# Optimization experiments

Hardware: AMD Instinct MI355X
Metric: run time of the kernel (lower is better)

Reference implementation:

```python
import jax, jax.numpy as jnp
import numpy as np

B, C, H = 16, 256, 32          # batch, in_channels(=out_channels), image_size
HEADS, HS = 8, 32              # heads = out_channels // head_size
D = HEADS * HS                 # head_dim = 256
N = H * H                      # tokens = 1024
EPS = 1e-5


def _rel_indices(h, w):
    # Faithful port of RelativeAttention2d.get_indices
    y = np.arange(h)
    x = np.arange(w)
    y1, x1, y2, x2 = np.meshgrid(y, x, y, x, indexing='ij')
    idx = (y1 - y2 + h - 1) * (2 * w - 1) + (x1 - x2 + w - 1)
    return jnp.asarray(idx.reshape(-1), dtype=jnp.int32)  # [N*N]


def setup_inputs() -> dict:
    key = jax.random.key(0)
    ks = jax.random.split(key, 10)
    s = 0.02
    return {
        'x': jax.random.normal(ks[0], (B, C, H, H), jnp.float32),
        'ln_g': jnp.ones((C,), jnp.float32),
        'ln_b': jnp.zeros((C,), jnp.float32),
        'wq': jax.random.normal(ks[1], (D, C), jnp.float32) * s,
        'bq': jnp.zeros((D,), jnp.float32),
        'wk': jax.random.normal(ks[2], (D, C), jnp.float32) * s,
        'bk': jnp.zeros((D,), jnp.float32),
        'wv': jax.random.normal(ks[3], (D, C), jnp.float32) * s,
        'bv': jnp.zeros((D,), jnp.float32),
        'wo': jax.random.normal(ks[4], (C, D), jnp.float32) * s,
        'bo': jnp.zeros((C,), jnp.float32),
        'rel_bias': jax.random.normal(ks[5], (HEADS, (2 * H - 1) * (2 * H - 1)), jnp.float32),
        'rel_idx': _rel_indices(H, H),
    }


def reference(x, ln_g, ln_b, wq, bq, wk, bk, wv, bv, wo, bo, rel_bias, rel_idx):
    b = x.shape[0]
    # norm(): LayerNorm over channel axis (dim 1 after the double transpose)
    mu = jnp.mean(x, axis=1, keepdims=True)
    var = jnp.mean((x - mu) ** 2, axis=1, keepdims=True)
    xn = (x - mu) / jnp.sqrt(var + EPS)
    xn = xn * ln_g[None, :, None, None] + ln_b[None, :, None, None]
    # reshape_for_linear: raw reshape [b, C, H, W] -> [b, N, C] (as in torch)
    xr = xn.reshape(b, N, C)
    # projections, then raw view(b, heads, head_size, -1) as in torch
    q = (xr @ wq.T + bq).reshape(b, HEADS, HS, N)
    k = (xr @ wk.T + bk).reshape(b, HEADS, HS, N)
    v = (xr @ wv.T + bv).reshape(b, HEADS, HS, N)
    # dots = k^T q / sqrt(head_dim)   [b, heads, N, N]
    dots = jnp.einsum('bhdn,bhdm->bhnm', k, q) / np.float32(np.sqrt(D))
    # gathered relative position bias  [heads, N, N]
    bias = rel_bias[:, rel_idx].reshape(HEADS, N, N)
    attn = jax.nn.softmax(dots + bias[None], axis=-2)  # non-standard softmax dim
    # out = v @ attn  [b, heads, head_size, N]
    out = jnp.einsum('bhdn,bhnm->bhdm', v, attn)
    out = out.reshape(b, H, H, D)  # raw view as in torch
    out = out @ wo.T + bo          # to_output linear (dropout is identity in eval)
    out = out.reshape(b, C, H, H)  # raw view back to [b, out_channels, H, W]
    return x + out
```

## Files before the change

### kernel.cpp

```cpp
#include <hip/hip_runtime.h>
#include <cstdint>

#define PERB 262144

typedef __attribute__((ext_vector_type(8))) short bf16x8;
typedef __attribute__((ext_vector_type(4))) float f32x4;
typedef unsigned short ushort_t;

__device__ __forceinline__ uint16_t f2bf(float f) {
    uint32_t u = __float_as_uint(f);
    u += 0x7fff + ((u >> 16) & 1);
    return (uint16_t)(u >> 16);
}

__global__ __launch_bounds__(256) void wcvt_kernel(
    const float* __restrict__ wq, const float* __restrict__ wk,
    const float* __restrict__ wv, const float* __restrict__ wo,
    ushort_t* __restrict__ oq, ushort_t* __restrict__ ok,
    ushort_t* __restrict__ ov, ushort_t* __restrict__ oo)
{
    const int which = blockIdx.x >> 6;
    const int idx = ((blockIdx.x & 63) * 256 + threadIdx.x) * 4;
    const float* src = which == 0 ? wq : which == 1 ? wk : which == 2 ? wv : wo;
    ushort_t* dst    = which == 0 ? oq : which == 1 ? ok : which == 2 ? ov : oo;
    const float4 v = *(const float4*)&src[idx];
    uint2 p;
    p.x = (uint32_t)f2bf(v.x) | ((uint32_t)f2bf(v.y) << 16);
    p.y = (uint32_t)f2bf(v.z) | ((uint32_t)f2bf(v.w) << 16);
    *(uint2*)&dst[idx] = p;
}

__global__ __launch_bounds__(256) void ln_kernel(
    const float* __restrict__ x, const float* __restrict__ gam,
    const float* __restrict__ bet, ushort_t* __restrict__ X)
{
    const int blk = blockIdx.x;
    const int b   = blk >> 4;
    const int sp0 = (blk & 15) << 6;
    const int tid = threadIdx.x;
    const int spl = tid & 63;
    const int cg  = tid >> 6;
    const int c0  = cg << 6;
    const int sp  = sp0 + spl;
    const float* xb = x + (size_t)b * PERB + sp;

    float vals[64];
    float s = 0.f, sq = 0.f;
#pragma unroll
    for (int i = 0; i < 64; ++i) {
        float v = xb[(size_t)(c0 + i) * 1024];
        vals[i] = v; s += v; sq += v * v;
    }
    __shared__ float rs[4][64];
    __shared__ float rq[4][64];
    rs[cg][spl] = s; rq[cg][spl] = sq;
    __syncthreads();
    const float ts = rs[0][spl] + rs[1][spl] + rs[2][spl] + rs[3][spl];
    const float tq = rq[0][spl] + rq[1][spl] + rq[2][spl] + rq[3][spl];
    const float mean = ts * (1.f / 256.f);
    const float var  = tq * (1.f / 256.f) - mean * mean;
    const float rstd = rsqrtf(var + 1e-5f);

    ushort_t* Xb = X + (size_t)b * PERB + sp;
#pragma unroll
    for (int i = 0; i < 64; ++i) {
        const int c = c0 + i;
        Xb[(size_t)c * 1024] = f2bf((vals[i] - mean) * rstd * gam[c] + bet[c]);
    }
}

__global__ __launch_bounds__(256, 3) void qkv_kernel(
    const ushort_t* __restrict__ X,
    const ushort_t* __restrict__ wq, const float* __restrict__ bq,
    const ushort_t* __restrict__ wk, const float* __restrict__ bk,
    const ushort_t* __restrict__ wv, const float* __restrict__ bv,
    ushort_t* __restrict__ Q, ushort_t* __restrict__ K, ushort_t* __restrict__ V)
{
    __shared__ __align__(16) ushort_t Xl[512 * 8];
    __shared__ __align__(16) ushort_t Wl[3][512 * 8];

    const int blk = blockIdx.x;
    const int m0  = (blk >> 2) << 6;
    const int n0  = (blk & 3) << 6;
    const int tid = threadIdx.x;
    const int w    = tid >> 6;
    const int lane = tid & 63;
    const int quad = lane >> 4;
    const int c    = lane & 15;

    f32x4 acc[3][4];
#pragma unroll
    for (int o3 = 0; o3 < 3; ++o3)
#pragma unroll
        for (int i = 0; i < 4; ++i) acc[o3][i] = (f32x4){0.f, 0.f, 0.f, 0.f};

    for (int kc = 0; kc < 4; ++kc) {
        const int k0 = kc << 6;
        __syncthreads();
#pragma unroll
        for (int i = 0; i < 2; ++i) {
            const int id = tid + i * 256;
            const int kq = id >> 6, m = id & 63;
            *(bf16x8*)&Xl[id * 8] = *(const bf16x8*)&X[(size_t)(m0 + m) * 256 + k0 + kq * 8];
        }
#pragma unroll
        for (int i = 0; i < 2; ++i) {
            const int id = tid + i * 256;
            const int kq = id >> 6, n = id & 63;
            const size_t g = (size_t)(n0 + n) * 256 + k0 + kq * 8;
            *(bf16x8*)&Wl[0][id * 8] = *(const bf16x8*)&wq[g];
            *(bf16x8*)&Wl[1][id * 8] = *(const bf16x8*)&wk[g];
            *(bf16x8*)&Wl[2][id * 8] = *(const bf16x8*)&wv[g];
        }
        __syncthreads();
#pragma unroll
        for (int ks = 0; ks < 2; ++ks) {
            const int kq = ks * 4 + quad;
            bf16x8 af[4];
#pragma unroll
            for (int msub = 0; msub < 4; ++msub)
                af[msub] = *(const bf16x8*)&Xl[(kq * 64 + msub * 16 + c) * 8];
            bf16x8 bw[3];
#pragma unroll
            for (int o3 = 0; o3 < 3; ++o3)
                bw[o3] = *(const bf16x8*)&Wl[o3][(kq * 64 + w * 16 + c) * 8];
#pragma unroll
            for (int o3 = 0; o3 < 3; ++o3)
#pragma unroll
                for (int msub = 0; msub < 4; ++msub)
                    acc[o3][msub] = __builtin_amdgcn_mfma_f32_16x16x32_bf16(
                        bw[o3], af[msub], acc[o3][msub], 0, 0, 0);
        }
    }

    const int n = n0 + w * 16 + quad * 4;
    const float4 bq4 = *(const float4*)&bq[n];
    const float4 bk4 = *(const float4*)&bk[n];
    const float4 bv4 = *(const float4*)&bv[n];
    ushort_t* outs[3] = {Q, K, V};
    const float4 bias[3] = {bq4, bk4, bv4};
#pragma unroll
    for (int msub = 0; msub < 4; ++msub) {
        const size_t m = (size_t)(m0 + msub * 16 + c);
#pragma unroll
        for (int o3 = 0; o3 < 3; ++o3) {
            const f32x4 a = acc[o3][msub];
            uint2 p;
            p.x = (uint32_t)f2bf(a[0] + bias[o3].x) | ((uint32_t)f2bf(a[1] + bias[o3].y) << 16);
            p.y = (uint32_t)f2bf(a[2] + bias[o3].z) | ((uint32_t)f2bf(a[3] + bias[o3].w) << 16);
            *(uint2*)&outs[o3][m * 256 + n] = p;
        }
    }
}

#define C1F 0.09016844005556022f
#define LOG2EF 1.4426950408889634f

__global__ __launch_bounds__(256, 4) void attn_kernel(
    const ushort_t* __restrict__ Q, const ushort_t* __restrict__ K,
    const ushort_t* __restrict__ V, const float* __restrict__ relb,
    ushort_t* __restrict__ O)
{
    __shared__ __align__(16) unsigned char smem[28672];
    char* Pb = (char*)smem;
    char* Kl = (char*)(smem + 16384);
    char* Vl = (char*)(smem + 20480);

    const int blk = blockIdx.x;
    const int bh  = blk & 127;
    const int mt  = blk >> 7;
    const int b   = bh >> 3;
    const int h   = bh & 7;
    const int m0  = mt << 7;
    const int tid = threadIdx.x;
    const int w    = tid >> 6;
    const int lane = tid & 63;
    const int quad = lane >> 4;
    const int c    = lane & 15;

    const size_t base = (size_t)b * PERB + (size_t)h * 32768;
    const ushort_t* Qg = Q + base;
    const ushort_t* Kg = K + base;
    const ushort_t* Vg = V + base;
    const float* rbh = relb + h * 3969;

    {
        const int mm = tid & 127;
        const int sg = tid >> 7;
        union { bf16x8 v; uint16_t u[8]; } g0, g1;
#pragma unroll
        for (int j = 0; j < 8; ++j)
            g0.u[j] = Qg[(size_t)(sg * 16 + j) * 1024 + m0 + mm];
#pragma unroll
        for (int j = 0; j < 8; ++j)
            g1.u[j] = Qg[(size_t)(sg * 16 + 8 + j) * 1024 + m0 + mm];
        *(bf16x8*)(Pb + (sg * 2 + 0) * 2048 + mm * 16) = g0.v;
        *(bf16x8*)(Pb + (sg * 2 + 1) * 2048 + mm * 16) = g1.v;
    }
    __syncthreads();
    bf16x8 qfrag[8];
#pragma unroll
    for (int msub = 0; msub < 8; ++msub)
        qfrag[msub] = *(const bf16x8*)(Pb + quad * 2048 + (msub * 16 + c) * 16);

    int moff[8];
#pragma unroll
    for (int msub = 0; msub < 8; ++msub) {
        const int m = m0 + msub * 16 + c;
        moff[msub] = 1984 - (m >> 5) * 63 - (m & 31);
    }

    f32x4 oacc[2][2], dacc[2];
#pragma unroll
    for (int i = 0; i < 2; ++i) {
        dacc[i] = (f32x4){0.f, 0.f, 0.f, 0.f};
#pragma unroll
        for (int j = 0; j < 2; ++j) oacc[i][j] = (f32x4){0.f, 0.f, 0.f, 0.f};
    }
    bf16x8 onesf;
#pragma unroll
    for (int j = 0; j < 8; ++j) onesf[j] = (short)0x3F80;

    const int knn = tid & 63, ksg = tid >> 6;
    const int vs  = tid >> 3, vng = tid & 7;
    const int kWr = ksg * 1024 + knn * 16;
    const int vWr = vs * 128 + ((vng ^ (vs & 7)) << 4);
    const int kRd = quad * 1024 + (w * 16 + c) * 16;
    const int pWr = c * 128 + (((2 * w + (quad >> 1)) ^ (c & 7)) << 4) + ((quad & 1) << 3);
    const int c7  = c & 7;

    uint32_t kpre[8]; bf16x8 vpre;
#pragma unroll
    for (int j = 0; j < 8; ++j) kpre[j] = Kg[(size_t)(ksg * 8 + j) * 1024 + knn];
    vpre = *(const bf16x8*)&Vg[(size_t)vs * 1024 + vng * 8];

    for (int ch = 0; ch < 16; ++ch) {
        const int n0c = ch << 6;
        const int cb  = ch & 1;

        {
            uint4 kp;
            kp.x = kpre[0] | (kpre[1] << 16);
            kp.y = kpre[2] | (kpre[3] << 16);
            kp.z = kpre[4] | (kpre[5] << 16);
            kp.w = kpre[6] | (kpre[7] << 16);
            *(uint4*)(Kl + kWr) = kp;
            *(bf16x8*)(Vl + cb * 4096 + vWr) = vpre;
        }
        __syncthreads();

        {
            const int n0n = ((ch + 1) & 15) << 6;
#pragma unroll
            for (int j = 0; j < 8; ++j)
                kpre[j] = Kg[(size_t)(ksg * 8 + j) * 1024 + n0n + knn];
            vpre = *(const bf16x8*)&Vg[(size_t)vs * 1024 + n0n + vng * 8];
        }

        const bf16x8 kf = *(const bf16x8*)(Kl + kRd);
        f32x4 sacc[8];
#pragma unroll
        for (int msub = 0; msub < 8; ++msub) {
            const f32x4 z = {0.f, 0.f, 0.f, 0.f};
            sacc[msub] = __builtin_amdgcn_mfma_f32_16x16x32_bf16(kf, qfrag[msub], z, 0, 0, 0);
        }

        const int nbase = n0c + w * 16 + quad * 4;
        const int nidx0 = (nbase >> 5) * 63 + (nbase & 31);
#pragma unroll
        for (int msub = 0; msub < 8; ++msub) {
            const float* bp = rbh + nidx0 + moff[msub];
            float p[4];
#pragma unroll
            for (int r = 0; r < 4; ++r)
                p[r] = __builtin_amdgcn_exp2f(fmaf(bp[r], LOG2EF, sacc[msub][r] * C1F));
            uint2 pk;
            pk.x = __builtin_amdgcn_perm(__float_as_uint(p[1]), __float_as_uint(p[0]), 0x07060302u);
            pk.y = __builtin_amdgcn_perm(__float_as_uint(p[3]), __float_as_uint(p[2]), 0x07060302u);
            *(uint2*)(Pb + msub * 2048 + pWr) = pk;
        }
        __syncthreads();

#pragma unroll
        for (int kstep = 0; kstep < 2; ++kstep) {
            const int u = ((kstep * 4 + quad) ^ c7) << 4;
            const bf16x8 vf0 = *(const bf16x8*)(Vl + cb * 4096 + c * 128 + u);
            const bf16x8 vf1 = *(const bf16x8*)(Vl + cb * 4096 + (16 + c) * 128 + u);
#pragma unroll
            for (int mi = 0; mi < 2; ++mi) {
                const bf16x8 pf = *(const bf16x8*)(Pb + ((w * 2 + mi) * 16 + c) * 128 + u);
                oacc[0][mi] = __builtin_amdgcn_mfma_f32_16x16x32_bf16(vf0, pf, oacc[0][mi], 0, 0, 0);
                oacc[1][mi] = __builtin_amdgcn_mfma_f32_16x16x32_bf16(vf1, pf, oacc[1][mi], 0, 0, 0);
                dacc[mi]    = __builtin_amdgcn_mfma_f32_16x16x32_bf16(onesf, pf, dacc[mi], 0, 0, 0);
            }
        }
    }

    ushort_t* Ob = O + base;
#pragma unroll
    for (int mi = 0; mi < 2; ++mi) {
        const float inv = 1.0f / dacc[mi][0];
        const int m = m0 + (w * 2 + mi) * 16 + c;
#pragma unroll
        for (int ssub = 0; ssub < 2; ++ssub)
#pragma unroll
            for (int r = 0; r < 4; ++r)
                Ob[(size_t)(ssub * 16 + quad * 4 + r) * 1024 + m] = f2bf(oacc[ssub][mi][r] * inv);
    }
}

__global__ __launch_bounds__(256, 4) void oproj_kernel(
    const ushort_t* __restrict__ A, const ushort_t* __restrict__ wo,
    const float* __restrict__ bo, const float* __restrict__ x,
    float* __restrict__ out)
{
    __shared__ __align__(16) ushort_t Al[512 * 8];
    __shared__ __align__(16) ushort_t Wl[512 * 8];

    const int blk = blockIdx.x;
    const int m0  = (blk >> 2) << 6;
    const int n0  = (blk & 3) << 6;
    const int tid = threadIdx.x;
    const int w    = tid >> 6;
    const int lane = tid & 63;
    const int quad = lane >> 4;
    const int c    = lane & 15;

    f32x4 acc[4];
#pragma unroll
    for (int i = 0; i < 4; ++i) acc[i] = (f32x4){0.f, 0.f, 0.f, 0.f};

    for (int kc = 0; kc < 4; ++kc) {
        const int k0 = kc << 6;
        __syncthreads();
#pragma unroll
        for (int i = 0; i < 2; ++i) {
            const int id = tid + i * 256;
            const int kq = id >> 6, mn = id & 63;
            *(bf16x8*)&Al[id * 8] = *(const bf16x8*)&A [(size_t)(m0 + mn) * 256 + k0 + kq * 8];
            *(bf16x8*)&Wl[id * 8] = *(const bf16x8*)&wo[(size_t)(n0 + mn) * 256 + k0 + kq * 8];
        }
        __syncthreads();
#pragma unroll
        for (int ks = 0; ks < 2; ++ks) {
            const int kq = ks * 4 + quad;
            const bf16x8 bw = *(const bf16x8*)&Wl[(kq * 64 + w * 16 + c) * 8];
#pragma unroll
            for (int msub = 0; msub < 4; ++msub) {
                const bf16x8 af = *(const bf16x8*)&Al[(kq * 64 + msub * 16 + c) * 8];
                acc[msub] = __builtin_amdgcn_mfma_f32_16x16x32_bf16(bw, af, acc[msub], 0, 0, 0);
            }
        }
    }

    const int n = n0 + w * 16 + quad * 4;
    const float4 bo4 = *(const float4*)&bo[n];
#pragma unroll
    for (int msub = 0; msub < 4; ++msub) {
        const size_t g = (size_t)(m0 + msub * 16 + c) * 256 + n;
        const float4 r = *(const float4*)&x[g];
        float4 t;
        t.x = acc[msub][0] + bo4.x + r.x;
        t.y = acc[msub][1] + bo4.y + r.y;
        t.z = acc[msub][2] + bo4.z + r.z;
        t.w = acc[msub][3] + bo4.w + r.w;
        *(float4*)&out[g] = t;
    }
}

extern "C" void kernel_launch(void* const* d_in, const int* in_sizes, int n_in,
                              void* d_out, int out_size, void* d_ws, size_t ws_size,
                              hipStream_t stream)
{
    (void)in_sizes; (void)n_in; (void)out_size; (void)ws_size;
    const float* x   = (const float*)d_in[0];
    const float* lng = (const float*)d_in[1];
    const float* lnb = (const float*)d_in[2];
    const float* wq  = (const float*)d_in[3];
    const float* bq  = (const float*)d_in[4];
    const float* wk  = (const float*)d_in[5];
    const float* bk  = (const float*)d_in[6];
    const float* wv  = (const float*)d_in[7];
    const float* bv  = (const float*)d_in[8];
    const float* wo  = (const float*)d_in[9];
    const float* bo  = (const float*)d_in[10];
    const float* rb  = (const float*)d_in[11];

    ushort_t* ws = (ushort_t*)d_ws;
    ushort_t* Xbf = ws;
    ushort_t* Qbf = ws + 1 * 4194304;
    ushort_t* Kbf = ws + 2 * 4194304;
    ushort_t* Vbf = ws + 3 * 4194304;
    ushort_t* Obf = ws + 4 * 4194304;
    ushort_t* Wqb = ws + 5 * 4194304;
    ushort_t* Wkb = Wqb + 65536;
    ushort_t* Wvb = Wkb + 65536;
    ushort_t* Wob = Wvb + 65536;
    float* out = (float*)d_out;

    hipLaunchKernelGGL(wcvt_kernel,  dim3(256),  dim3(256), 0, stream,
                       wq, wk, wv, wo, Wqb, Wkb, Wvb, Wob);
    hipLaunchKernelGGL(ln_kernel,    dim3(256),  dim3(256), 0, stream, x, lng, lnb, Xbf);
    hipLaunchKernelGGL(qkv_kernel,   dim3(1024), dim3(256), 0, stream,
                       Xbf, Wqb, bq, Wkb, bk, Wvb, bv, Qbf, Kbf, Vbf);
    hipLaunchKernelGGL(attn_kernel,  dim3(1024), dim3(256), 0, stream, Qbf, Kbf, Vbf, rb, Obf);
    hipLaunchKernelGGL(oproj_kernel, dim3(1024), dim3(256), 0, stream, Obf, Wob, bo, x, out);
}
```

Measured before the change: 175.7 us.

## Vectorize LayerNorm and drop LDS staging in QKV and output projection GEMMs

LayerNorm now uses 512 blocks. Each thread loads float4 spans of four spatial positions over eight channels, reduces across 32 channel groups in shared memory, and writes ushort4. This targets more memory-level parallelism and wider accesses. The QKV and output projection GEMMs no longer stage tiles through LDS with barriers. Each wave loads its MFMA operands straight from global memory (relying on cache reuse), which removes the syncs and LDS traffic but adds redundant global loads. The QKV kernel's occupancy hint rises from 3 to 4.

```diff
diff --git a/kernel.cpp b/kernel.cpp
--- a/kernel.cpp
+++ b/kernel.cpp
@@ -30,55 +30,72 @@
     *(uint2*)&dst[idx] = p;
 }
 
-__global__ __launch_bounds__(256) void ln_kernel(
+__global__ __launch_bounds__(256, 4) void ln_kernel(
     const float* __restrict__ x, const float* __restrict__ gam,
     const float* __restrict__ bet, ushort_t* __restrict__ X)
 {
     const int blk = blockIdx.x;
-    const int b   = blk >> 4;
-    const int sp0 = (blk & 15) << 6;
+    const int b   = blk >> 5;
+    const int sp0 = (blk & 31) << 5;
     const int tid = threadIdx.x;
-    const int spl = tid & 63;
-    const int cg  = tid >> 6;
-    const int c0  = cg << 6;
-    const int sp  = sp0 + spl;
-    const float* xb = x + (size_t)b * PERB + sp;
-
-    float vals[64];
-    float s = 0.f, sq = 0.f;
-#pragma unroll
-    for (int i = 0; i < 64; ++i) {
-        float v = xb[(size_t)(c0 + i) * 1024];
-        vals[i] = v; s += v; sq += v * v;
-    }
-    __shared__ float rs[4][64];
-    __shared__ float rq[4][64];
-    rs[cg][spl] = s; rq[cg][spl] = sq;
+    const int spI = tid & 7;
+    const int cgI = tid >> 3;
+    const int c0  = cgI << 3;
+    const size_t xoff = (size_t)b * PERB + sp0 + spI * 4;
+    const float* xb = x + xoff;
+
+    float4 v[8];
+    float4 s4  = make_float4(0.f, 0.f, 0.f, 0.f);
+    float4 q4  = make_float4(0.f, 0.f, 0.f, 0.f);
+#pragma unroll
+    for (int i = 0; i < 8; ++i) {
+        v[i] = *(const float4*)&xb[(size_t)(c0 + i) * 1024];
+        s4.x += v[i].x; s4.y += v[i].y; s4.z += v[i].z; s4.w += v[i].w;
+        q4.x += v[i].x * v[i].x; q4.y += v[i].y * v[i].y;
+        q4.z += v[i].z * v[i].z; q4.w += v[i].w * v[i].w;
+    }
+    __shared__ __align__(16) float4 rs[32][8];
+    __shared__ __align__(16) float4 rq[32][8];
+    rs[cgI][spI] = s4; rq[cgI][spI] = q4;
     __syncthreads();
-    const float ts = rs[0][spl] + rs[1][spl] + rs[2][spl] + rs[3][spl];
-    const float tq = rq[0][spl] + rq[1][spl] + rq[2][spl] + rq[3][spl];
-    const float mean = ts * (1.f / 256.f);
-    const float var  = tq * (1.f / 256.f) - mean * mean;
-    const float rstd = rsqrtf(var + 1e-5f);
-
-    ushort_t* Xb = X + (size_t)b * PERB + sp;
-#pragma unroll
-    for (int i = 0; i < 64; ++i) {
+    float4 ts = make_float4(0.f, 0.f, 0.f, 0.f);
+    float4 tq = make_float4(0.f, 0.f, 0.f, 0.f);
+#pragma unroll
+    for (int j = 0; j < 32; ++j) {
+        const float4 a = rs[j][spI];
+        const float4 bqq = rq[j][spI];
+        ts.x += a.x; ts.y += a.y; ts.z += a.z; ts.w += a.w;
+        tq.x += bqq.x; tq.y += bqq.y; tq.z += bqq.z; tq.w += bqq.w;
+    }
+    float4 mean, rstd;
+    mean.x = ts.x * (1.f / 256.f); mean.y = ts.y * (1.f / 256.f);
+    mean.z = ts.z * (1.f / 256.f); mean.w = ts.w * (1.f / 256.f);
+    rstd.x = rsqrtf(tq.x * (1.f / 256.f) - mean.x * mean.x + 1e-5f);
+    rstd.y = rsqrtf(tq.y * (1.f / 256.f) - mean.y * mean.y + 1e-5f);
+    rstd.z = rsqrtf(tq.z * (1.f / 256.f) - mean.z * mean.z + 1e-5f);
+    rstd.w = rsqrtf(tq.w * (1.f / 256.f) - mean.w * mean.w + 1e-5f);
+
+    ushort_t* Xb = X + xoff;
+#pragma unroll
+    for (int i = 0; i < 8; ++i) {
         const int c = c0 + i;
-        Xb[(size_t)c * 1024] = f2bf((vals[i] - mean) * rstd * gam[c] + bet[c]);
-    }
-}
-
-__global__ __launch_bounds__(256, 3) void qkv_kernel(
+        const float g = gam[c], be = bet[c];
+        ushort4 o;
+        o.x = f2bf((v[i].x - mean.x) * rstd.x * g + be);
+        o.y = f2bf((v[i].y - mean.y) * rstd.y * g + be);
+        o.z = f2bf((v[i].z - mean.z) * rstd.z * g + be);
+        o.w = f2bf((v[i].w - mean.w) * rstd.w * g + be);
+        *(ushort4*)&Xb[(size_t)c * 1024] = o;
+    }
+}
+
+__global__ __launch_bounds__(256, 4) void qkv_kernel(
     const ushort_t* __restrict__ X,
     const ushort_t* __restrict__ wq, const float* __restrict__ bq,
     const ushort_t* __restrict__ wk, const float* __restrict__ bk,
     const ushort_t* __restrict__ wv, const float* __restrict__ bv,
     ushort_t* __restrict__ Q, ushort_t* __restrict__ K, ushort_t* __restrict__ V)
 {
-    __shared__ __align__(16) ushort_t Xl[512 * 8];
-    __shared__ __align__(16) ushort_t Wl[3][512 * 8];
-
     const int blk = blockIdx.x;
     const int m0  = (blk >> 2) << 6;
     const int n0  = (blk & 3) << 6;
@@ -88,49 +105,37 @@
     const int quad = lane >> 4;
     const int c    = lane & 15;
 
+    const ushort_t* Arow[4];
+#pragma unroll
+    for (int msub = 0; msub < 4; ++msub)
+        Arow[msub] = X + (size_t)(m0 + msub * 16 + c) * 256 + quad * 8;
+    const size_t woff = (size_t)(n0 + w * 16 + c) * 256 + quad * 8;
+    const ushort_t* Bq = wq + woff;
+    const ushort_t* Bk = wk + woff;
+    const ushort_t* Bv = wv + woff;
+
     f32x4 acc[3][4];
 #pragma unroll
     for (int o3 = 0; o3 < 3; ++o3)
 #pragma unroll
         for (int i = 0; i < 4; ++i) acc[o3][i] = (f32x4){0.f, 0.f, 0.f, 0.f};
 
-    for (int kc = 0; kc < 4; ++kc) {
-        const int k0 = kc << 6;
-        __syncthreads();
-#pragma unroll
-        for (int i = 0; i < 2; ++i) {
-            const int id = tid + i * 256;
-            const int kq = id >> 6, m = id & 63;
-            *(bf16x8*)&Xl[id * 8] = *(const bf16x8*)&X[(size_t)(m0 + m) * 256 + k0 + kq * 8];
-        }
-#pragma unroll
-        for (int i = 0; i < 2; ++i) {
-            const int id = tid + i * 256;
-            const int kq = id >> 6, n = id & 63;
-            const size_t g = (size_t)(n0 + n) * 256 + k0 + kq * 8;
-            *(bf16x8*)&Wl[0][id * 8] = *(const bf16x8*)&wq[g];
-            *(bf16x8*)&Wl[1][id * 8] = *(const bf16x8*)&wk[g];
-            *(bf16x8*)&Wl[2][id * 8] = *(const bf16x8*)&wv[g];
-        }
-        __syncthreads();
-#pragma unroll
-        for (int ks = 0; ks < 2; ++ks) {
-            const int kq = ks * 4 + quad;
-            bf16x8 af[4];
+#pragma unroll
+    for (int kstep = 0; kstep < 8; ++kstep) {
+        const int ko = kstep * 32;
+        bf16x8 af[4], bw[3];
+#pragma unroll
+        for (int msub = 0; msub < 4; ++msub)
+            af[msub] = *(const bf16x8*)(Arow[msub] + ko);
+        bw[0] = *(const bf16x8*)(Bq + ko);
+        bw[1] = *(const bf16x8*)(Bk + ko);
+        bw[2] = *(const bf16x8*)(Bv + ko);
+#pragma unroll
+        for (int o3 = 0; o3 < 3; ++o3)
 #pragma unroll
             for (int msub = 0; msub < 4; ++msub)
-                af[msub] = *(const bf16x8*)&Xl[(kq * 64 + msub * 16 + c) * 8];
-            bf16x8 bw[3];
-#pragma unroll
-            for (int o3 = 0; o3 < 3; ++o3)
-                bw[o3] = *(const bf16x8*)&Wl[o3][(kq * 64 + w * 16 + c) * 8];
-#pragma unroll
-            for (int o3 = 0; o3 < 3; ++o3)
-#pragma unroll
-                for (int msub = 0; msub < 4; ++msub)
-                    acc[o3][msub] = __builtin_amdgcn_mfma_f32_16x16x32_bf16(
-                        bw[o3], af[msub], acc[o3][msub], 0, 0, 0);
-        }
+                acc[o3][msub] = __builtin_amdgcn_mfma_f32_16x16x32_bf16(
+                    bw[o3], af[msub], acc[o3][msub], 0, 0, 0);
     }
 
     const int n = n0 + w * 16 + quad * 4;
@@ -314,9 +319,6 @@
     const float* __restrict__ bo, const float* __restrict__ x,
     float* __restrict__ out)
 {
-    __shared__ __align__(16) ushort_t Al[512 * 8];
-    __shared__ __align__(16) ushort_t Wl[512 * 8];
-
     const int blk = blockIdx.x;
     const int m0  = (blk >> 2) << 6;
     const int n0  = (blk & 3) << 6;
@@ -326,30 +328,24 @@
     const int quad = lane >> 4;
     const int c    = lane & 15;
 
+    const ushort_t* Arow[4];
+#pragma unroll
+    for (int msub = 0; msub < 4; ++msub)
+        Arow[msub] = A + (size_t)(m0 + msub * 16 + c) * 256 + quad * 8;
+    const ushort_t* Bw = wo + (size_t)(n0 + w * 16 + c) * 256 + quad * 8;
+
     f32x4 acc[4];
 #pragma unroll
     for (int i = 0; i < 4; ++i) acc[i] = (f32x4){0.f, 0.f, 0.f, 0.f};
 
-    for (int kc = 0; kc < 4; ++kc) {
-        const int k0 = kc << 6;
-        __syncthreads();
-#pragma unroll
-        for (int i = 0; i < 2; ++i) {
-            const int id = tid + i * 256;
-            const int kq = id >> 6, mn = id & 63;
-            *(bf16x8*)&Al[id * 8] = *(const bf16x8*)&A [(size_t)(m0 + mn) * 256 + k0 + kq * 8];
-            *(bf16x8*)&Wl[id * 8] = *(const bf16x8*)&wo[(size_t)(n0 + mn) * 256 + k0 + kq * 8];
-        }
-        __syncthreads();
-#pragma unroll
-        for (int ks = 0; ks < 2; ++ks) {
-            const int kq = ks * 4 + quad;
-            const bf16x8 bw = *(const bf16x8*)&Wl[(kq * 64 + w * 16 + c) * 8];
-#pragma unroll
-            for (int msub = 0; msub < 4; ++msub) {
-                const bf16x8 af = *(const bf16x8*)&Al[(kq * 64 + msub * 16 + c) * 8];
-                acc[msub] = __builtin_amdgcn_mfma_f32_16x16x32_bf16(bw, af, acc[msub], 0, 0, 0);
-            }
+#pragma unroll
+    for (int kstep = 0; kstep < 8; ++kstep) {
+        const int ko = kstep * 32;
+        const bf16x8 bw = *(const bf16x8*)(Bw + ko);
+#pragma unroll
+        for (int msub = 0; msub < 4; ++msub) {
+            const bf16x8 af = *(const bf16x8*)(Arow[msub] + ko);
+            acc[msub] = __builtin_amdgcn_mfma_f32_16x16x32_bf16(bw, af, acc[msub], 0, 0, 0);
         }
     }
 
@@ -400,7 +396,7 @@
 
     hipLaunchKernelGGL(wcvt_kernel,  dim3(256),  dim3(256), 0, stream,
                        wq, wk, wv, wo, Wqb, Wkb, Wvb, Wob);
-    hipLaunchKernelGGL(ln_kernel,    dim3(256),  dim3(256), 0, stream, x, lng, lnb, Xbf);
+    hipLaunchKernelGGL(ln_kernel,    dim3(512),  dim3(256), 0, stream, x, lng, lnb, Xbf);
     hipLaunchKernelGGL(qkv_kernel,   dim3(1024), dim3(256), 0, stream,
                        Xbf, Wqb, bq, Wkb, bk, Wvb, bv, Qbf, Kbf, Vbf);
     hipLaunchKernelGGL(attn_kernel,  dim3(1024), dim3(256), 0, stream, Qbf, Kbf, Vbf, rb, Obf);
```

New measurement: 189.5 us. 1.08x slower.
